# Kernel optimization log

Hardware: AMD Instinct MI355X
Metric: run time of the kernel (lower is better)

Reference implementation:

```python
import jax, jax.numpy as jnp
import numpy as np
from jax import lax

R = 4                 # radius (init kwarg)
EPS = 2.0             # eps (init kwarg)
K = 2 * R + 1         # stencil size


def _dir_kernels():
    """8 directional box kernels [8,1,K,K]: L,R,U,D,NW,NE,SW,SE (matches torch construction)."""
    base = np.ones((K, K), np.float32)
    L = base.copy(); L[:, R + 1:] = 0
    Rk = base.copy(); Rk[:, :R] = 0
    U = base.copy(); U[R + 1:, :] = 0
    D = base.copy(); D[:R, :] = 0
    NW = U.copy(); NE = U.copy(); SW = D.copy(); SE = D.copy()
    half = float((R + 1) * (2 * R + 1))
    L, Rk, U, D = L / half, Rk / half, U / half, D / half
    NW[:, R + 1:] = 0; NE[:, :R] = 0; SW[:, R + 1:] = 0; SE[:, :R] = 0
    quad = float((R + 1) ** 2)
    NW, NE, SW, SE = NW / quad, NE / quad, SW / quad, SE / quad
    return jnp.asarray(np.stack([L, Rk, U, D, NW, NE, SW, SE])[:, None])


def _pad(x):
    # ReplicationPad2d(R)
    return jnp.pad(x, ((0, 0), (0, 0), (R, R), (R, R)), mode='edge')


def _conv(x, w, groups=1):
    return lax.conv_general_dilated(
        x, w, window_strides=(1, 1), padding='VALID',
        dimension_numbers=('NCHW', 'OIHW', 'NCHW'), feature_group_count=groups)


def _resize_bilinear_ac(x, H, W):
    """Bilinear resize with align_corners=True, separable gather. x: [N,C,h,w]."""
    n, c, h, w = x.shape
    dt = x.dtype

    def coords(out, src):
        t = jnp.arange(out, dtype=dt) * (jnp.asarray(src - 1, dt) / jnp.asarray(out - 1, dt))
        i0 = jnp.clip(jnp.floor(t).astype(jnp.int32), 0, src - 2)
        f = t - i0.astype(dt)
        return i0, f

    y0, fy = coords(H, h)
    x0, fx = coords(W, w)
    rows = x[:, :, y0, :] * (1 - fy)[None, None, :, None] + x[:, :, y0 + 1, :] * fy[None, None, :, None]
    return rows[:, :, :, x0] * (1 - fx) + rows[:, :, :, x0 + 1] * fx


def setup_inputs() -> dict:
    key = jax.random.key(0)
    k1, k2, k3 = jax.random.split(key, 3)
    lr_x = jax.random.uniform(k1, (1, 3, 256, 256), jnp.float32) * 255.0
    lr_y = jax.random.uniform(k2, (1, 3, 256, 256), jnp.float32) * 255.0
    hr_x = jax.random.uniform(k3, (1, 3, 1024, 1024), jnp.float32) * 255.0
    box_w = jnp.full((3, 1, K, K), 1.0 / (K * K), jnp.float32)  # depthwise box filter weights
    return {"lr_x": lr_x, "lr_y": lr_y, "hr_x": hr_x, "box_w": box_w}


def reference(lr_x, lr_y, hr_x, box_w):
    H, W = hr_x.shape[2], hr_x.shape[3]
    box = lambda t: _conv(_pad(t), box_w, groups=3)

    # --- guided filter coefficients at low res ---
    mean_x = box(lr_x)
    mean_y = box(lr_y)
    cov_xy = box(lr_x * lr_y) - mean_x * mean_y
    var_x = box(lr_x * lr_x) - mean_x * mean_x
    A = cov_xy / (var_x + EPS)
    b = mean_y - A * mean_x

    # --- upsample A, b to hr (bilinear, align_corners=True) ---
    A = _resize_bilinear_ac(A, H, W)
    b = _resize_bilinear_ac(b, H, W)

    # --- 8-direction side-window stencil; channels treated as batch ---
    dirw = _dir_kernels()                      # [8,1,K,K]
    A3 = _pad(A.reshape(3, 1, H, W))
    b3 = _pad(b.reshape(3, 1, H, W))
    im3 = hr_x.reshape(3, 1, H, W)
    cA = _conv(A3, dirw)                       # [3,8,H,W]
    cB = _conv(b3, dirw)                       # [3,8,H,W]
    d = cA * im3 + cB - im3                    # [3,8,H,W]

    idx = jnp.argmin(jnp.abs(d), axis=1, keepdims=True)
    dm = jnp.take_along_axis(d, idx, axis=1)   # min-|delta| direction
    res = (dm + im3).reshape(1, 3, H, W)

    # res.int() truncates toward zero, then clamp(0,255), then float
    return jnp.clip(jnp.trunc(res), 0.0, 255.0)
```

## Files before the change

kernel.cpp:

```cpp
#include <hip/hip_runtime.h>

#define RR 4
#define LRN 256
#define HRN 1024
#define SCALE (255.0f/1023.0f)

#define TX 32
#define TYR 64
#define BTH 8
#define NROW (TYR / BTH)
#define LRC 12
#define LRR 20
#define GC (LRC + 8)
#define GR (LRR + 8)

typedef float v2 __attribute__((ext_vector_type(2)));

__device__ inline int anchor_of(int u) {
    int k = min(max(u - 4, 0), HRN - 1);
    float t = (float)k * SCALE;
    int i = (int)t; if (i > LRN - 2) i = LRN - 2;
    return i;
}

__device__ inline float4 mkw(int k0, int k1, int a) {
    float4 w = make_float4(0.f, 0.f, 0.f, 0.f);
    for (int k = k0; k <= k1; ++k) {
        int kc = min(max(k, 0), HRN - 1);
        float t = (float)kc * SCALE;
        int i = (int)t; if (i > LRN - 2) i = LRN - 2;
        float f = t - (float)i;
        int off = i - a;
        float wa = 1.0f - f, wb = f;
        w.x += (off == 0) ? wa : 0.0f;
        w.y += (off == 1) ? wa : ((off == 0) ? wb : 0.0f);
        w.z += (off == 2) ? wa : ((off == 1) ? wb : 0.0f);
        w.w += (off == 2) ? wb : 0.0f;
    }
    return w;
}

__global__ __launch_bounds__(256, 6) void fused_kernel(
    const float* __restrict__ lrx, const float* __restrict__ lry,
    const float* __restrict__ hrx, float* __restrict__ out)
{
    __shared__ alignas(16) char region1[18432];
    float4 (*sV)[GC]  = reinterpret_cast<float4(*)[GC]>(region1);
    float4 (*sHS)[LRC] = reinterpret_cast<float4(*)[LRC]>(region1 + GR * GC * 16);
    v2 (*sT)[LRC]  = reinterpret_cast<v2(*)[LRC]>(region1);
    v2 (*sBm)[LRC] = reinterpret_cast<v2(*)[LRC]>(region1 + 6144);
    v2 (*sF)[LRC]  = reinterpret_cast<v2(*)[LRC]>(region1 + 12288);

    __shared__ v2     sAB[LRR][LRC];
    __shared__ float4 sYW[TYR][3];
    __shared__ int    sYA[TYR];
    __shared__ float4 sXW[TX][3];
    __shared__ int    sXA[TX];

    const int c  = blockIdx.z;
    const int X0 = blockIdx.x * TX, Y0 = blockIdx.y * TYR;
    const int tid = threadIdx.y * TX + threadIdx.x;
    const float* px = lrx + c * LRN * LRN;
    const float* py = lry + c * LRN * LRN;

    const int rowbase = anchor_of(Y0);
    const int colbase = anchor_of(X0);

    if (tid < TX) {
        int x = X0 + tid;
        int a = anchor_of(x);
        sXA[tid] = a - colbase;
        sXW[tid][0] = mkw(x - 4, x,     a);
        sXW[tid][1] = mkw(x,     x + 4, a);
        sXW[tid][2] = mkw(x - 4, x + 4, a);
    } else if (tid >= 64 && tid < 64 + TYR) {
        int r = tid - 64;
        int y = Y0 + r;
        int a = anchor_of(y);
        sYA[r] = a - rowbase;
        sYW[r][0] = mkw(y - 4, y,     a);
        sYW[r][1] = mkw(y,     y + 4, a);
        sYW[r][2] = mkw(y - 4, y + 4, a);
    }

    for (int i = tid; i < GR * GC; i += 256) {
        int r = i / GC, cc = i - r * GC;
        int gy = min(max(rowbase - 4 + r, 0), LRN - 1);
        int gx = min(max(colbase - 4 + cc, 0), LRN - 1);
        float xv = px[gy * LRN + gx];
        float yv = py[gy * LRN + gx];
        sV[r][cc] = make_float4(xv, yv, xv * yv, xv * xv);
    }
    __syncthreads();

    for (int i = tid; i < GR * LRC; i += 256) {
        int r = i / LRC, cc = i - r * LRC;
        float4 s = sV[r][cc];
        #pragma unroll
        for (int k = 1; k < 9; ++k) {
            float4 v = sV[r][cc + k];
            s.x += v.x; s.y += v.y; s.z += v.z; s.w += v.w;
        }
        sHS[r][cc] = s;
    }
    __syncthreads();

    for (int i = tid; i < LRR * LRC; i += 256) {
        int r = i / LRC, cc = i - r * LRC;
        float4 s = sHS[r][cc];
        #pragma unroll
        for (int k = 1; k < 9; ++k) {
            float4 v = sHS[r + k][cc];
            s.x += v.x; s.y += v.y; s.z += v.z; s.w += v.w;
        }
        const float inv81 = 1.0f / 81.0f;
        float mx = s.x * inv81, my = s.y * inv81;
        float cov = s.z * inv81 - mx * my;
        float var = s.w * inv81 - mx * mx;
        float A = cov / (var + 2.0f);
        float B = my - A * mx;
        v2 ab; ab.x = A; ab.y = B;
        sAB[r][cc] = ab;
    }
    __syncthreads();

    for (int i = tid; i < TYR * LRC; i += 256) {
        int r = i / LRC, cc = i - r * LRC;
        int ra = sYA[r];
        float4 wT = sYW[r][0], wB = sYW[r][1], wF = sYW[r][2];
        v2 v0 = sAB[ra][cc],     v1 = sAB[ra + 1][cc];
        v2 v2_ = sAB[ra + 2][cc], v3 = sAB[ra + 3][cc];
        v2 t, b, f;
        t = v0 * wT.x; t = __builtin_elementwise_fma((v2)(wT.y), v1, t);
        t = __builtin_elementwise_fma((v2)(wT.z), v2_, t);
        t = __builtin_elementwise_fma((v2)(wT.w), v3, t);
        b = v0 * wB.x; b = __builtin_elementwise_fma((v2)(wB.y), v1, b);
        b = __builtin_elementwise_fma((v2)(wB.z), v2_, b);
        b = __builtin_elementwise_fma((v2)(wB.w), v3, b);
        f = v0 * wF.x; f = __builtin_elementwise_fma((v2)(wF.y), v1, f);
        f = __builtin_elementwise_fma((v2)(wF.z), v2_, f);
        f = __builtin_elementwise_fma((v2)(wF.w), v3, f);
        sT[r][cc] = t; sBm[r][cc] = b; sF[r][cc] = f;
    }
    __syncthreads();

    const int tx = threadIdx.x, tyw = threadIdx.y;
    const int c0 = sXA[tx];
    const float4 wL = sXW[tx][0], wR = sXW[tx][1], wFh = sXW[tx][2];
    const float i45 = 1.0f / 45.0f, i25 = 1.0f / 25.0f;
    const float* hp = hrx + (c * HRN + Y0 + tyw) * HRN + X0 + tx;
    float*       op = out + (c * HRN + Y0 + tyw) * HRN + X0 + tx;

    #pragma unroll
    for (int j = 0; j < NROW; ++j) {
        const int r = tyw + j * BTH;
        v2 aL = 0, aR = 0, aU = 0, aD = 0;
        v2 aNW = 0, aNE = 0, aSW = 0, aSE = 0;
        #pragma unroll
        for (int k = 0; k < 4; ++k) {
            float wl = (k==0)?wL.x:(k==1)?wL.y:(k==2)?wL.z:wL.w;
            float wr = (k==0)?wR.x:(k==1)?wR.y:(k==2)?wR.z:wR.w;
            float wf = (k==0)?wFh.x:(k==1)?wFh.y:(k==2)?wFh.z:wFh.w;
            v2 tv = sT[r][c0 + k];
            v2 bv = sBm[r][c0 + k];
            v2 fv = sF[r][c0 + k];
            aL  = __builtin_elementwise_fma((v2)(wl), fv, aL);
            aR  = __builtin_elementwise_fma((v2)(wr), fv, aR);
            aU  = __builtin_elementwise_fma((v2)(wf), tv, aU);
            aD  = __builtin_elementwise_fma((v2)(wf), bv, aD);
            aNW = __builtin_elementwise_fma((v2)(wl), tv, aNW);
            aNE = __builtin_elementwise_fma((v2)(wr), tv, aNE);
            aSW = __builtin_elementwise_fma((v2)(wl), bv, aSW);
            aSE = __builtin_elementwise_fma((v2)(wr), bv, aSE);
        }
        float xv = hp[j * BTH * HRN];

        float d0 = fmaf(i45, fmaf(aL.x,  xv, aL.y),  -xv);
        float d1 = fmaf(i45, fmaf(aR.x,  xv, aR.y),  -xv);
        float d2 = fmaf(i45, fmaf(aU.x,  xv, aU.y),  -xv);
        float d3 = fmaf(i45, fmaf(aD.x,  xv, aD.y),  -xv);
        float d4 = fmaf(i25, fmaf(aNW.x, xv, aNW.y), -xv);
        float d5 = fmaf(i25, fmaf(aNE.x, xv, aNE.y), -xv);
        float d6 = fmaf(i25, fmaf(aSW.x, xv, aSW.y), -xv);
        float d7 = fmaf(i25, fmaf(aSE.x, xv, aSE.y), -xv);

        float a0 = fabsf(d0), a1 = fabsf(d1), a2 = fabsf(d2), a3 = fabsf(d3);
        float a4 = fabsf(d4), a5 = fabsf(d5), a6 = fabsf(d6), a7 = fabsf(d7);
        bool c01 = a0 <= a1; float w01 = c01 ? d0 : d1; float m01 = c01 ? a0 : a1;
        bool c23 = a2 <= a3; float w23 = c23 ? d2 : d3; float m23 = c23 ? a2 : a3;
        bool c45 = a4 <= a5; float w45 = c45 ? d4 : d5; float m45 = c45 ? a4 : a5;
        bool c67 = a6 <= a7; float w67 = c67 ? d6 : d7; float m67 = c67 ? a6 : a7;
        bool cA_ = m01 <= m23; float wA = cA_ ? w01 : w23; float mA = cA_ ? m01 : m23;
        bool cB_ = m45 <= m67; float wB_ = cB_ ? w45 : w67; float mB = cB_ ? m45 : m67;
        float bd = (mA <= mB) ? wA : wB_;

        float res = __builtin_amdgcn_fmed3f(truncf(bd + xv), 0.0f, 255.0f);
        op[j * BTH * HRN] = res;
    }
}

extern "C" void kernel_launch(void* const* d_in, const int* in_sizes, int n_in,
                              void* d_out, int out_size, void* d_ws, size_t ws_size,
                              hipStream_t stream) {
    const float* lrx = (const float*)d_in[0];
    const float* lry = (const float*)d_in[1];
    const float* hrx = (const float*)d_in[2];
    (void)d_in[3]; (void)in_sizes; (void)n_in; (void)out_size;
    (void)d_ws; (void)ws_size;

    float* outp = (float*)d_out;
    dim3 block(TX, BTH);
    dim3 grid(HRN / TX, HRN / TYR, 3);
    fused_kernel<<<grid, block, 0, stream>>>(lrx, lry, hrx, outp);
}
```

Measured before the change: 84.38 us.

## Split fused kernel into low-res coefficient pass and high-res stencil pass

```diff
diff --git a/kernel.cpp b/kernel.cpp
--- a/kernel.cpp
+++ b/kernel.cpp
@@ -5,16 +5,10 @@
 #define HRN 1024
 #define SCALE (255.0f/1023.0f)
 
-#define TX 32
-#define TYR 64
-#define BTH 8
-#define NROW (TYR / BTH)
-#define LRC 12
-#define LRR 20
-#define GC (LRC + 8)
-#define GR (LRR + 8)
-
 typedef float v2 __attribute__((ext_vector_type(2)));
+
+#define WS_LUTW 4096
+#define WS_AB   65536
 
 __device__ inline int anchor_of(int u) {
     int k = min(max(u - 4, 0), HRN - 1);
@@ -40,61 +34,41 @@
     return w;
 }
 
-__global__ __launch_bounds__(256, 6) void fused_kernel(
+__global__ __launch_bounds__(256, 4) void lr_kernel(
     const float* __restrict__ lrx, const float* __restrict__ lry,
-    const float* __restrict__ hrx, float* __restrict__ out)
+    float* __restrict__ ws)
 {
-    __shared__ alignas(16) char region1[18432];
-    float4 (*sV)[GC]  = reinterpret_cast<float4(*)[GC]>(region1);
-    float4 (*sHS)[LRC] = reinterpret_cast<float4(*)[LRC]>(region1 + GR * GC * 16);
-    v2 (*sT)[LRC]  = reinterpret_cast<v2(*)[LRC]>(region1);
-    v2 (*sBm)[LRC] = reinterpret_cast<v2(*)[LRC]>(region1 + 6144);
-    v2 (*sF)[LRC]  = reinterpret_cast<v2(*)[LRC]>(region1 + 12288);
-
-    __shared__ v2     sAB[LRR][LRC];
-    __shared__ float4 sYW[TYR][3];
-    __shared__ int    sYA[TYR];
-    __shared__ float4 sXW[TX][3];
-    __shared__ int    sXA[TX];
+    __shared__ float4 sV[24][40];
+    __shared__ float4 sHS[24][32];
 
     const int c  = blockIdx.z;
-    const int X0 = blockIdx.x * TX, Y0 = blockIdx.y * TYR;
-    const int tid = threadIdx.y * TX + threadIdx.x;
+    const int X0 = blockIdx.x * 32, Y0 = blockIdx.y * 16;
+    const int tid = threadIdx.y * 32 + threadIdx.x;
     const float* px = lrx + c * LRN * LRN;
     const float* py = lry + c * LRN * LRN;
 
-    const int rowbase = anchor_of(Y0);
-    const int colbase = anchor_of(X0);
-
-    if (tid < TX) {
-        int x = X0 + tid;
-        int a = anchor_of(x);
-        sXA[tid] = a - colbase;
-        sXW[tid][0] = mkw(x - 4, x,     a);
-        sXW[tid][1] = mkw(x,     x + 4, a);
-        sXW[tid][2] = mkw(x - 4, x + 4, a);
-    } else if (tid >= 64 && tid < 64 + TYR) {
-        int r = tid - 64;
-        int y = Y0 + r;
-        int a = anchor_of(y);
-        sYA[r] = a - rowbase;
-        sYW[r][0] = mkw(y - 4, y,     a);
-        sYW[r][1] = mkw(y,     y + 4, a);
-        sYW[r][2] = mkw(y - 4, y + 4, a);
-    }
-
-    for (int i = tid; i < GR * GC; i += 256) {
-        int r = i / GC, cc = i - r * GC;
-        int gy = min(max(rowbase - 4 + r, 0), LRN - 1);
-        int gx = min(max(colbase - 4 + cc, 0), LRN - 1);
+    if (c == 0 && blockIdx.y == 0 && tid < 128) {
+        int u = blockIdx.x * 128 + tid;
+        int a = anchor_of(u);
+        ((int*)ws)[u] = a;
+        float4* w = (float4*)((char*)ws + WS_LUTW) + u * 3;
+        w[0] = mkw(u - 4, u,     a);
+        w[1] = mkw(u,     u + 4, a);
+        w[2] = mkw(u - 4, u + 4, a);
+    }
+
+    for (int i = tid; i < 24 * 40; i += 256) {
+        int r = i / 40, cc = i - r * 40;
+        int gy = min(max(Y0 - 4 + r, 0), LRN - 1);
+        int gx = min(max(X0 - 4 + cc, 0), LRN - 1);
         float xv = px[gy * LRN + gx];
         float yv = py[gy * LRN + gx];
         sV[r][cc] = make_float4(xv, yv, xv * yv, xv * xv);
     }
     __syncthreads();
 
-    for (int i = tid; i < GR * LRC; i += 256) {
-        int r = i / LRC, cc = i - r * LRC;
+    for (int i = tid; i < 24 * 32; i += 256) {
+        int r = i / 32, cc = i & 31;
         float4 s = sV[r][cc];
         #pragma unroll
         for (int k = 1; k < 9; ++k) {
@@ -105,8 +79,9 @@
     }
     __syncthreads();
 
-    for (int i = tid; i < LRR * LRC; i += 256) {
-        int r = i / LRC, cc = i - r * LRC;
+    v2* ab_out = (v2*)((char*)ws + WS_AB);
+    for (int i = tid; i < 16 * 32; i += 256) {
+        int r = i / 32, cc = i & 31;
         float4 s = sHS[r][cc];
         #pragma unroll
         for (int k = 1; k < 9; ++k) {
@@ -120,7 +95,58 @@
         float A = cov / (var + 2.0f);
         float B = my - A * mx;
         v2 ab; ab.x = A; ab.y = B;
-        sAB[r][cc] = ab;
+        ab_out[(c * LRN + (Y0 + r)) * LRN + X0 + cc] = ab;
+    }
+}
+
+#define TX 32
+#define TYR 32
+#define BTH 8
+#define NROW (TYR / BTH)
+#define LRC 12
+#define LRR 12
+
+__global__ __launch_bounds__(256, 7) void hr_kernel(
+    const float* __restrict__ hrx, const float* __restrict__ ws,
+    float* __restrict__ out)
+{
+    __shared__ float4 sTB[TYR][LRC];
+    __shared__ v2     sF[TYR][LRC];
+    __shared__ v2     sAB[LRR][LRC];
+    __shared__ float4 sYW[TYR][3];
+    __shared__ int    sYA[TYR];
+    __shared__ float4 sXW[TX][3];
+    __shared__ int    sXA[TX];
+
+    const int c  = blockIdx.z;
+    const int X0 = blockIdx.x * TX, Y0 = blockIdx.y * TYR;
+    const int tid = threadIdx.y * TX + threadIdx.x;
+
+    const int*    lutA = (const int*)ws;
+    const float4* lutW = (const float4*)((const char*)ws + WS_LUTW);
+    const v2*     AB   = (const v2*)((const char*)ws + WS_AB) + c * LRN * LRN;
+
+    const int rowbase = lutA[Y0];
+    const int colbase = lutA[X0];
+
+    if (tid < TX) {
+        int u = X0 + tid;
+        sXA[tid] = lutA[u] - colbase;
+        sXW[tid][0] = lutW[u * 3 + 0];
+        sXW[tid][1] = lutW[u * 3 + 1];
+        sXW[tid][2] = lutW[u * 3 + 2];
+    } else if (tid >= 64 && tid < 64 + TYR) {
+        int r = tid - 64, u = Y0 + r;
+        sYA[r] = lutA[u] - rowbase;
+        sYW[r][0] = lutW[u * 3 + 0];
+        sYW[r][1] = lutW[u * 3 + 1];
+        sYW[r][2] = lutW[u * 3 + 2];
+    } else if (tid >= 96 && tid < 96 + LRR * LRC) {
+        int i = tid - 96;
+        int r = i / LRC, cc = i - r * LRC;
+        int gy = min(rowbase + r, LRN - 1);
+        int gx = min(colbase + cc, LRN - 1);
+        sAB[r][cc] = AB[gy * LRN + gx];
     }
     __syncthreads();
 
@@ -140,7 +166,8 @@
         f = v0 * wF.x; f = __builtin_elementwise_fma((v2)(wF.y), v1, f);
         f = __builtin_elementwise_fma((v2)(wF.z), v2_, f);
         f = __builtin_elementwise_fma((v2)(wF.w), v3, f);
-        sT[r][cc] = t; sBm[r][cc] = b; sF[r][cc] = f;
+        sTB[r][cc] = make_float4(t.x, t.y, b.x, b.y);
+        sF[r][cc]  = f;
     }
     __syncthreads();
 
@@ -161,8 +188,9 @@
             float wl = (k==0)?wL.x:(k==1)?wL.y:(k==2)?wL.z:wL.w;
             float wr = (k==0)?wR.x:(k==1)?wR.y:(k==2)?wR.z:wR.w;
             float wf = (k==0)?wFh.x:(k==1)?wFh.y:(k==2)?wFh.z:wFh.w;
-            v2 tv = sT[r][c0 + k];
-            v2 bv = sBm[r][c0 + k];
+            float4 tb = sTB[r][c0 + k];
+            v2 tv; tv.x = tb.x; tv.y = tb.y;
+            v2 bv; bv.x = tb.z; bv.y = tb.w;
             v2 fv = sF[r][c0 + k];
             aL  = __builtin_elementwise_fma((v2)(wl), fv, aL);
             aR  = __builtin_elementwise_fma((v2)(wr), fv, aR);
@@ -205,11 +233,11 @@
     const float* lrx = (const float*)d_in[0];
     const float* lry = (const float*)d_in[1];
     const float* hrx = (const float*)d_in[2];
-    (void)d_in[3]; (void)in_sizes; (void)n_in; (void)out_size;
-    (void)d_ws; (void)ws_size;
-
+    (void)d_in[3]; (void)in_sizes; (void)n_in; (void)out_size; (void)ws_size;
+
+    float* ws   = (float*)d_ws;
     float* outp = (float*)d_out;
-    dim3 block(TX, BTH);
-    dim3 grid(HRN / TX, HRN / TYR, 3);
-    fused_kernel<<<grid, block, 0, stream>>>(lrx, lry, hrx, outp);
-}
+
+    lr_kernel<<<dim3(LRN / 32, LRN / 16, 3), dim3(32, 8), 0, stream>>>(lrx, lry, ws);
+    hr_kernel<<<dim3(HRN / TX, HRN / TYR, 3), dim3(TX, BTH), 0, stream>>>(hrx, ws, outp);
+}
```

Measured after the change: 85.35 us. Within noise of the previous version (+1.1%).
